# Kernel tuning notes

Measured on AMD Instinct MI355X. Metric: run time of the kernel, lower is better.

The kernel has to match this reference:

```python
import jax, jax.numpy as jnp
import numpy as np

B = 65536
NREQ = 2097152
NVEH = 1048576
NPAS = 2097152
E = 4194304


def _xavier(key, fi, fo):
    gain = 5.0 / 3.0  # tanh gain
    std = gain * np.sqrt(2.0 / (fi + fo))
    return jax.random.normal(key, (fi, fo), dtype=jnp.float32) * std


def scatter_mean(x, idx, num_segments):
    s = jax.ops.segment_sum(x, idx, num_segments=num_segments)
    c = jax.ops.segment_sum(jnp.ones((x.shape[0], 1), x.dtype), idx, num_segments=num_segments)
    return s / jnp.maximum(c, 1.0)


def setup_inputs() -> dict:
    key = jax.random.key(0)
    ks = jax.random.split(key, 16)
    inp = {
        "requests_x": jax.random.normal(ks[0], (NREQ, 10), dtype=jnp.float32),
        "requests_x_batch": jnp.sort(jax.random.randint(ks[1], (NREQ,), 0, B)),
        "vehicles_x": jax.random.normal(ks[2], (NVEH, 8), dtype=jnp.float32),
        "vehicles_x_batch": jnp.sort(jax.random.randint(ks[3], (NVEH,), 0, B)),
        "passengers_x": jax.random.normal(ks[4], (NPAS, 10), dtype=jnp.float32),
        "veh2pas_receiver_edge_index": jax.random.randint(ks[5], (E,), 0, NPAS),
        "veh2pas_sender_edge_index": jax.random.randint(ks[6], (E,), 0, NVEH),
        "req2veh_receiver_start_index": jax.random.randint(ks[7], (B,), 0, NVEH),
        "W_req": _xavier(ks[8], 10, 16), "b_req": jnp.zeros((16,), jnp.float32),
        "W_veh": _xavier(ks[9], 8, 16), "b_veh": jnp.zeros((16,), jnp.float32),
        "W_pas": _xavier(ks[10], 10, 16), "b_pas": jnp.zeros((16,), jnp.float32),
        "W1": _xavier(ks[11], 64, 64), "b1": jnp.zeros((64,), jnp.float32),
        "W2": _xavier(ks[12], 64, 64), "b2": jnp.zeros((64,), jnp.float32),
        "W3": _xavier(ks[13], 64, 1), "b3": jnp.zeros((1,), jnp.float32),
    }
    return inp


def reference(requests_x, requests_x_batch, vehicles_x, vehicles_x_batch, passengers_x,
              veh2pas_receiver_edge_index, veh2pas_sender_edge_index,
              req2veh_receiver_start_index,
              W_req, b_req, W_veh, b_veh, W_pas, b_pas, W1, b1, W2, b2, W3, b3):
    # per-node-type small MLPs
    req_feat = jnp.tanh(requests_x @ W_req + b_req)            # [NREQ,16]
    req_mean = scatter_mean(req_feat, requests_x_batch, B)      # [B,16]
    veh_feat = jnp.tanh(vehicles_x @ W_veh + b_veh)             # [NVEH,16]
    pas_feat = jnp.tanh(passengers_x @ W_pas + b_pas)           # [NPAS,16]
    # gather passengers along edges, mean-pool onto vehicles
    pas_mean = scatter_mean(pas_feat[veh2pas_receiver_edge_index],
                            veh2pas_sender_edge_index, NVEH)    # [NVEH,16]
    ego_feat = jnp.concatenate([veh_feat, pas_mean], axis=-1)[req2veh_receiver_start_index]  # [B,32]
    veh_mean = scatter_mean(veh_feat, vehicles_x_batch, B)      # [B,16]
    action_feat = jnp.concatenate([req_mean, ego_feat, veh_mean], axis=-1)  # [B,64]
    h = jnp.tanh(action_feat @ W1 + b1)
    h = jnp.tanh(h @ W2 + b2)
    return h @ W3 + b3                                          # [B,1]
```

## Files before the change

kernel.cpp:

```cpp
#include <hip/hip_runtime.h>
#include <cstddef>
#include <cstdint>

#define TPB 256
#define BATCH 65536
#define NREQ 2097152
#define NVEH 1048576
#define NEDGE 4194304
#define CAP 32
#define RSENT 0xFFFFu

__device__ __forceinline__ float fast_tanh(float x) {
    float e = __expf(2.0f * x);
    return fmaf(-2.0f, __builtin_amdgcn_rcpf(e + 1.0f), 1.0f);
}
__device__ __forceinline__ float4 tanh4(float4 v) {
    return make_float4(fast_tanh(v.x), fast_tanh(v.y), fast_tanh(v.z), fast_tanh(v.w));
}

template<int F>
__device__ __forceinline__ void load_row(const float* __restrict__ x, int r, float* xr) {
    if constexpr (F == 10) {
        const float2* p = reinterpret_cast<const float2*>(x + (size_t)r * 10);
        #pragma unroll
        for (int i = 0; i < 5; ++i) { float2 t = p[i]; xr[2*i] = t.x; xr[2*i+1] = t.y; }
    } else {
        const float4* p = reinterpret_cast<const float4*>(x + (size_t)r * 8);
        float4 a = p[0], b = p[1];
        xr[0]=a.x; xr[1]=a.y; xr[2]=a.z; xr[3]=a.w;
        xr[4]=b.x; xr[5]=b.y; xr[6]=b.z; xr[7]=b.w;
    }
}

__global__ __launch_bounds__(TPB) void k_bounds(
    const int* __restrict__ req_batch, const int* __restrict__ veh_batch,
    const int* __restrict__ req2veh,
    int* __restrict__ seg_req, int* __restrict__ seg_veh,
    unsigned* __restrict__ markbits, unsigned short* __restrict__ rank16,
    int* __restrict__ cnt)
{
    int t = blockIdx.x * TPB + threadIdx.x;
    int i0 = t * 4;
    {
        int4 c = *reinterpret_cast<const int4*>(req_batch + i0);
        int prev = (i0 == 0) ? -1 : req_batch[i0 - 1];
        int vals[4] = {c.x, c.y, c.z, c.w};
        #pragma unroll
        for (int u = 0; u < 4; ++u) {
            for (int b = prev + 1; b <= vals[u]; ++b) seg_req[b] = i0 + u;
            prev = vals[u];
        }
        if (i0 + 4 == NREQ)
            for (int b = prev + 1; b <= BATCH; ++b) seg_req[b] = NREQ;
    }
    if (i0 < NVEH) {
        int4 c = *reinterpret_cast<const int4*>(veh_batch + i0);
        int prev = (i0 == 0) ? -1 : veh_batch[i0 - 1];
        int vals[4] = {c.x, c.y, c.z, c.w};
        #pragma unroll
        for (int u = 0; u < 4; ++u) {
            for (int b = prev + 1; b <= vals[u]; ++b) seg_veh[b] = i0 + u;
            prev = vals[u];
        }
        if (i0 + 4 == NVEH)
            for (int b = prev + 1; b <= BATCH; ++b) seg_veh[b] = NVEH;
    }
    if (i0 < BATCH) {
        int4 vv = *reinterpret_cast<const int4*>(req2veh + i0);
        int vs[4] = {vv.x, vv.y, vv.z, vv.w};
        #pragma unroll
        for (int u = 0; u < 4; ++u) {
            int v = vs[u];
            unsigned bit = 1u << (v & 31);
            unsigned old = atomicOr(&markbits[v >> 5], bit);
            if (!(old & bit))
                rank16[v] = (unsigned short)atomicAdd(cnt, 1);
        }
    }
}

template<int F>
__device__ __forceinline__ void seg_mean_reg(
    const float* __restrict__ x, const int* __restrict__ seg,
    const float* __restrict__ W, const float* __restrict__ bias,
    float* __restrict__ mean_out, int b, int q)
{
    float4 wq[F];
    #pragma unroll
    for (int i = 0; i < F; ++i)
        wq[i] = *reinterpret_cast<const float4*>(&W[i*16 + q*4]);
    float4 bq = reinterpret_cast<const float4*>(bias)[q];

    int lo = seg[b];
    int hi = seg[b + 1];
    float4 s = make_float4(0.f, 0.f, 0.f, 0.f);

    int r = lo;
    for (; r + 4 <= hi; r += 4) {
        float xr[4][F];
        #pragma unroll
        for (int u = 0; u < 4; ++u) load_row<F>(x, r + u, xr[u]);
        #pragma unroll
        for (int u = 0; u < 4; ++u) {
            float4 acc = bq;
            #pragma unroll
            for (int i = 0; i < F; ++i) {
                acc.x = fmaf(xr[u][i], wq[i].x, acc.x);
                acc.y = fmaf(xr[u][i], wq[i].y, acc.y);
                acc.z = fmaf(xr[u][i], wq[i].z, acc.z);
                acc.w = fmaf(xr[u][i], wq[i].w, acc.w);
            }
            float4 tv = tanh4(acc);
            s.x += tv.x; s.y += tv.y; s.z += tv.z; s.w += tv.w;
        }
    }
    for (; r < hi; ++r) {
        float xr[F];
        load_row<F>(x, r, xr);
        float4 acc = bq;
        #pragma unroll
        for (int i = 0; i < F; ++i) {
            acc.x = fmaf(xr[i], wq[i].x, acc.x);
            acc.y = fmaf(xr[i], wq[i].y, acc.y);
            acc.z = fmaf(xr[i], wq[i].z, acc.z);
            acc.w = fmaf(xr[i], wq[i].w, acc.w);
        }
        float4 tv = tanh4(acc);
        s.x += tv.x; s.y += tv.y; s.z += tv.z; s.w += tv.w;
    }
    float inv = 1.0f / fmaxf((float)(hi - lo), 1.0f);
    float4 o = make_float4(s.x*inv, s.y*inv, s.z*inv, s.w*inv);
    reinterpret_cast<float4*>(mean_out)[(size_t)b*4 + q] = o;
}

__global__ __launch_bounds__(TPB, 4) void k_phase1(
    const float* __restrict__ requests_x, const int* __restrict__ seg_req,
    const float* __restrict__ vehicles_x, const int* __restrict__ seg_veh,
    const float* __restrict__ W_req, const float* __restrict__ b_req,
    const float* __restrict__ W_veh, const float* __restrict__ b_veh,
    float* __restrict__ req_mean, float* __restrict__ veh_mean)
{
    int blk = blockIdx.x, tid = threadIdx.x;
    if (blk < 1024) {
        int t = blk * TPB + tid;
        seg_mean_reg<10>(requests_x, seg_req, W_req, b_req, req_mean, t >> 2, t & 3);
    } else {
        int t = (blk - 1024) * TPB + tid;
        seg_mean_reg<8>(vehicles_x, seg_veh, W_veh, b_veh, veh_mean, t >> 2, t & 3);
    }
}

__global__ void k_edge(
    const int* __restrict__ send, const int* __restrict__ recv,
    const unsigned short* __restrict__ rank16,
    int* __restrict__ deg, int* __restrict__ bucket)
{
    int e4 = blockIdx.x * TPB + threadIdx.x;
    int4 sv = reinterpret_cast<const int4*>(send)[e4];
    int vv[4] = {sv.x, sv.y, sv.z, sv.w};
    unsigned rr[4];
    #pragma unroll
    for (int u = 0; u < 4; ++u) rr[u] = rank16[vv[u]];
    #pragma unroll
    for (int u = 0; u < 4; ++u) {
        if (rr[u] != RSENT) {
            int slot = atomicAdd(&deg[rr[u]], 1);
            if (slot < CAP) bucket[(size_t)rr[u] * CAP + slot] = recv[e4 * 4 + u];
        }
    }
}

__global__ __launch_bounds__(TPB, 3) void k_final(
    const float* __restrict__ req_mean, const float* __restrict__ veh_mean,
    const unsigned short* __restrict__ rank16, const int* __restrict__ deg,
    const int* __restrict__ bucket, const float* __restrict__ pas_x,
    const float* __restrict__ vehicles_x, const int* __restrict__ req2veh,
    const float* __restrict__ W_veh, const float* __restrict__ b_veh,
    const float* __restrict__ W_pas, const float* __restrict__ b_pas,
    const float* __restrict__ W1, const float* __restrict__ b1,
    const float* __restrict__ W2, const float* __restrict__ b2,
    const float* __restrict__ W3, const float* __restrict__ b3,
    float* __restrict__ out)
{
    __shared__ __align__(16) float sW1[4096];
    __shared__ __align__(16) float sW2[4096];
    __shared__ float sW3[64];
    __shared__ float sb1[64];
    __shared__ float sb2[64];

    int tid = threadIdx.x;
    {
        const float4* s1 = reinterpret_cast<const float4*>(W1);
        const float4* s2 = reinterpret_cast<const float4*>(W2);
        float4* d1 = reinterpret_cast<float4*>(sW1);
        float4* d2 = reinterpret_cast<float4*>(sW2);
        for (int i = tid; i < 1024; i += TPB) { d1[i] = s1[i]; d2[i] = s2[i]; }
        if (tid < 64) { sW3[tid] = W3[tid]; sb1[tid] = b1[tid]; sb2[tid] = b2[tid]; }
    }
    __syncthreads();

    int q = tid & 3;
    int b = blockIdx.x * (TPB / 4) + (tid >> 2);
    int lane = tid & 63;
    int lbase = lane & ~3;

    float a[64];
    {
        const float4* rs = reinterpret_cast<const float4*>(req_mean) + (size_t)b*4;
        const float4* vs = reinterpret_cast<const float4*>(veh_mean) + (size_t)b*4;
        #pragma unroll
        for (int j4 = 0; j4 < 4; ++j4) {
            float4 t = rs[j4];
            a[4*j4+0]=t.x; a[4*j4+1]=t.y; a[4*j4+2]=t.z; a[4*j4+3]=t.w;
            float4 u = vs[j4];
            a[48+4*j4+0]=u.x; a[48+4*j4+1]=u.y; a[48+4*j4+2]=u.z; a[48+4*j4+3]=u.w;
        }
    }
    int v = req2veh[b];

    float4 fv;
    {
        float4 wv[8];
        #pragma unroll
        for (int i = 0; i < 8; ++i)
            wv[i] = *reinterpret_cast<const float4*>(&W_veh[i*16 + q*4]);
        float4 bv = reinterpret_cast<const float4*>(b_veh)[q];
        const float4* vp = reinterpret_cast<const float4*>(vehicles_x + (size_t)v*8);
        float4 t0 = vp[0], t1 = vp[1];
        float vx[8] = {t0.x,t0.y,t0.z,t0.w,t1.x,t1.y,t1.z,t1.w};
        float4 acc = bv;
        #pragma unroll
        for (int i = 0; i < 8; ++i) {
            acc.x = fmaf(vx[i], wv[i].x, acc.x); acc.y = fmaf(vx[i], wv[i].y, acc.y);
            acc.z = fmaf(vx[i], wv[i].z, acc.z); acc.w = fmaf(vx[i], wv[i].w, acc.w);
        }
        fv = tanh4(acc);
    }

    float4 fp;
    {
        float4 wp[10];
        #pragma unroll
        for (int i = 0; i < 10; ++i)
            wp[i] = *reinterpret_cast<const float4*>(&W_pas[i*16 + q*4]);
        float4 bp = reinterpret_cast<const float4*>(b_pas)[q];
        int rk = rank16[v];
        int d = deg[rk];
        int n = min(d, CAP);
        const int4* bk4 = reinterpret_cast<const int4*>(bucket + (size_t)rk * CAP);
        float4 ps = make_float4(0.f, 0.f, 0.f, 0.f);
        for (int c = 0; c * 4 < n; ++c) {
            int4 idx = bk4[c];
            int pv[4] = {idx.x, idx.y, idx.z, idx.w};
            int m = n - c * 4;
            float px[4][10];
            #pragma unroll
            for (int u = 0; u < 4; ++u) {
                if (u < m) {
                    const float2* pp = reinterpret_cast<const float2*>(pas_x + (size_t)pv[u] * 10);
                    #pragma unroll
                    for (int i = 0; i < 5; ++i) {
                        float2 t = pp[i]; px[u][2*i] = t.x; px[u][2*i+1] = t.y;
                    }
                }
            }
            #pragma unroll
            for (int u = 0; u < 4; ++u) {
                if (u < m) {
                    float4 acc = bp;
                    #pragma unroll
                    for (int i = 0; i < 10; ++i) {
                        acc.x = fmaf(px[u][i], wp[i].x, acc.x);
                        acc.y = fmaf(px[u][i], wp[i].y, acc.y);
                        acc.z = fmaf(px[u][i], wp[i].z, acc.z);
                        acc.w = fmaf(px[u][i], wp[i].w, acc.w);
                    }
                    float4 t = tanh4(acc);
                    ps.x += t.x; ps.y += t.y; ps.z += t.z; ps.w += t.w;
                }
            }
        }
        float inv = 1.0f / fmaxf((float)d, 1.0f);
        fp = make_float4(ps.x*inv, ps.y*inv, ps.z*inv, ps.w*inv);
    }

    #pragma unroll
    for (int src = 0; src < 4; ++src) {
        a[16+4*src+0] = __shfl(fv.x, lbase+src);
        a[16+4*src+1] = __shfl(fv.y, lbase+src);
        a[16+4*src+2] = __shfl(fv.z, lbase+src);
        a[16+4*src+3] = __shfl(fv.w, lbase+src);
        a[32+4*src+0] = __shfl(fp.x, lbase+src);
        a[32+4*src+1] = __shfl(fp.y, lbase+src);
        a[32+4*src+2] = __shfl(fp.z, lbase+src);
        a[32+4*src+3] = __shfl(fp.w, lbase+src);
    }

    const float4* W1v = reinterpret_cast<const float4*>(sW1);
    const float4* W2v = reinterpret_cast<const float4*>(sW2);

    float hq[16];
    {
        float4 acc[4];
        #pragma unroll
        for (int jj = 0; jj < 4; ++jj)
            acc[jj] = *reinterpret_cast<const float4*>(&sb1[q*16 + jj*4]);
        #pragma unroll
        for (int k = 0; k < 64; ++k) {
            float ak = a[k];
            #pragma unroll
            for (int jj = 0; jj < 4; ++jj) {
                float4 w = W1v[k*16 + q*4 + jj];
                acc[jj].x = fmaf(ak, w.x, acc[jj].x); acc[jj].y = fmaf(ak, w.y, acc[jj].y);
                acc[jj].z = fmaf(ak, w.z, acc[jj].z); acc[jj].w = fmaf(ak, w.w, acc[jj].w);
            }
        }
        #pragma unroll
        for (int jj = 0; jj < 4; ++jj) {
            float4 t = tanh4(acc[jj]);
            hq[4*jj+0]=t.x; hq[4*jj+1]=t.y; hq[4*jj+2]=t.z; hq[4*jj+3]=t.w;
        }
    }
    #pragma unroll
    for (int src = 0; src < 4; ++src)
        #pragma unroll
        for (int jj = 0; jj < 16; ++jj)
            a[src*16 + jj] = __shfl(hq[jj], lbase + src);

    float o;
    {
        float4 acc[4];
        #pragma unroll
        for (int jj = 0; jj < 4; ++jj)
            acc[jj] = *reinterpret_cast<const float4*>(&sb2[q*16 + jj*4]);
        #pragma unroll
        for (int k = 0; k < 64; ++k) {
            float ak = a[k];
            #pragma unroll
            for (int jj = 0; jj < 4; ++jj) {
                float4 w = W2v[k*16 + q*4 + jj];
                acc[jj].x = fmaf(ak, w.x, acc[jj].x); acc[jj].y = fmaf(ak, w.y, acc[jj].y);
                acc[jj].z = fmaf(ak, w.z, acc[jj].z); acc[jj].w = fmaf(ak, w.w, acc[jj].w);
            }
        }
        o = 0.0f;
        #pragma unroll
        for (int jj = 0; jj < 4; ++jj) {
            float4 t = tanh4(acc[jj]);
            o = fmaf(t.x, sW3[q*16+4*jj+0], o);
            o = fmaf(t.y, sW3[q*16+4*jj+1], o);
            o = fmaf(t.z, sW3[q*16+4*jj+2], o);
            o = fmaf(t.w, sW3[q*16+4*jj+3], o);
        }
    }
    o += __shfl_xor(o, 1);
    o += __shfl_xor(o, 2);
    if (q == 0) out[b] = o + b3[0];
}

extern "C" void kernel_launch(void* const* d_in, const int* in_sizes, int n_in,
                              void* d_out, int out_size, void* d_ws, size_t ws_size,
                              hipStream_t stream) {
    const float* requests_x = (const float*)d_in[0];
    const int*   req_batch  = (const int*)d_in[1];
    const float* vehicles_x = (const float*)d_in[2];
    const int*   veh_batch  = (const int*)d_in[3];
    const float* pas_x      = (const float*)d_in[4];
    const int*   recv       = (const int*)d_in[5];
    const int*   send       = (const int*)d_in[6];
    const int*   req2veh    = (const int*)d_in[7];
    const float* W_req = (const float*)d_in[8];
    const float* b_req = (const float*)d_in[9];
    const float* W_veh = (const float*)d_in[10];
    const float* b_veh = (const float*)d_in[11];
    const float* W_pas = (const float*)d_in[12];
    const float* b_pas = (const float*)d_in[13];
    const float* W1 = (const float*)d_in[14];
    const float* b1 = (const float*)d_in[15];
    const float* W2 = (const float*)d_in[16];
    const float* b2 = (const float*)d_in[17];
    const float* W3 = (const float*)d_in[18];
    const float* b3 = (const float*)d_in[19];
    float* out = (float*)d_out;

    char* ws = (char*)d_ws;
    float*          req_mean = (float*)         (ws + 0);
    float*          veh_mean = (float*)         (ws + (4u<<20));
    int*            seg_req  = (int*)           (ws + (8u<<20));
    int*            seg_veh  = (int*)           (ws + (9u<<20));
    unsigned*       markbits = (unsigned*)      (ws + (10u<<20));
    int*            deg      = (int*)           (ws + (10u<<20) + (128u<<10));
    int*            cnt      = (int*)           (ws + (10u<<20) + (384u<<10));
    unsigned short* rank16   = (unsigned short*)(ws + (11u<<20));
    int*            bucket   = (int*)           (ws + (13u<<20));

    hipMemsetAsync(markbits, 0, (388u<<10), stream);
    hipMemsetAsync(rank16, 0xFF, NVEH * sizeof(unsigned short), stream);

    k_bounds<<<NREQ/4/TPB, TPB, 0, stream>>>(
        req_batch, veh_batch, req2veh, seg_req, seg_veh, markbits, rank16, cnt);

    k_edge<<<NEDGE/(TPB*4), TPB, 0, stream>>>(send, recv, rank16, deg, bucket);

    k_phase1<<<2048, TPB, 0, stream>>>(
        requests_x, seg_req, vehicles_x, seg_veh,
        W_req, b_req, W_veh, b_veh, req_mean, veh_mean);

    k_final<<<BATCH*4/TPB, TPB, 0, stream>>>(
        req_mean, veh_mean, rank16, deg, bucket, pas_x,
        vehicles_x, req2veh, W_veh, b_veh, W_pas, b_pas,
        W1, b1, W2, b2, W3, b3, out);
}
```

Baseline: 152.3 us.

## Compute passenger features in edge kernel and store half-precision features in buckets

```diff
diff --git a/kernel.cpp b/kernel.cpp
--- a/kernel.cpp
+++ b/kernel.cpp
@@ -1,4 +1,5 @@
 #include <hip/hip_runtime.h>
+#include <hip/hip_fp16.h>
 #include <cstddef>
 #include <cstdint>
 
@@ -152,20 +153,52 @@
 
 __global__ void k_edge(
     const int* __restrict__ send, const int* __restrict__ recv,
+    const float* __restrict__ pas_x,
+    const float* __restrict__ W_pas, const float* __restrict__ b_pas,
     const unsigned short* __restrict__ rank16,
-    int* __restrict__ deg, int* __restrict__ bucket)
+    int* __restrict__ deg, __half* __restrict__ bucketF)
 {
-    int e4 = blockIdx.x * TPB + threadIdx.x;
-    int4 sv = reinterpret_cast<const int4*>(send)[e4];
-    int vv[4] = {sv.x, sv.y, sv.z, sv.w};
-    unsigned rr[4];
+    int tid = threadIdx.x;
+    int lane = tid & 63;
+    int lbase = lane & ~3;
+    int q = tid & 3;
+
+    float4 wq[10];
     #pragma unroll
-    for (int u = 0; u < 4; ++u) rr[u] = rank16[vv[u]];
+    for (int i = 0; i < 10; ++i)
+        wq[i] = *reinterpret_cast<const float4*>(&W_pas[i*16 + q*4]);
+    float4 bq = reinterpret_cast<const float4*>(b_pas)[q];
+
+    int e = blockIdx.x * TPB + tid;
+    int v = send[e];
+    unsigned rk = rank16[v];
+    int slot = -1;
+    if (rk != RSENT) slot = atomicAdd(&deg[rk], 1);
+    int p = (rk != RSENT && slot < CAP) ? recv[e] : -1;
+
     #pragma unroll
     for (int u = 0; u < 4; ++u) {
-        if (rr[u] != RSENT) {
-            int slot = atomicAdd(&deg[rr[u]], 1);
-            if (slot < CAP) bucket[(size_t)rr[u] * CAP + slot] = recv[e4 * 4 + u];
+        int pu = __shfl(p, lbase + u);
+        if (pu >= 0) {
+            unsigned rku = (unsigned)__shfl((int)rk, lbase + u);
+            int slotu = __shfl(slot, lbase + u);
+            float px[10];
+            const float2* pp = reinterpret_cast<const float2*>(pas_x + (size_t)pu * 10);
+            #pragma unroll
+            for (int i = 0; i < 5; ++i) { float2 t = pp[i]; px[2*i] = t.x; px[2*i+1] = t.y; }
+            float4 acc = bq;
+            #pragma unroll
+            for (int i = 0; i < 10; ++i) {
+                acc.x = fmaf(px[i], wq[i].x, acc.x);
+                acc.y = fmaf(px[i], wq[i].y, acc.y);
+                acc.z = fmaf(px[i], wq[i].z, acc.z);
+                acc.w = fmaf(px[i], wq[i].w, acc.w);
+            }
+            float4 t = tanh4(acc);
+            __half2* dst = reinterpret_cast<__half2*>(
+                bucketF + ((size_t)rku * CAP + slotu) * 16) + q * 2;
+            dst[0] = __floats2half2_rn(t.x, t.y);
+            dst[1] = __floats2half2_rn(t.z, t.w);
         }
     }
 }
@@ -173,10 +206,9 @@
 __global__ __launch_bounds__(TPB, 3) void k_final(
     const float* __restrict__ req_mean, const float* __restrict__ veh_mean,
     const unsigned short* __restrict__ rank16, const int* __restrict__ deg,
-    const int* __restrict__ bucket, const float* __restrict__ pas_x,
+    const __half* __restrict__ bucketF,
     const float* __restrict__ vehicles_x, const int* __restrict__ req2veh,
     const float* __restrict__ W_veh, const float* __restrict__ b_veh,
-    const float* __restrict__ W_pas, const float* __restrict__ b_pas,
     const float* __restrict__ W1, const float* __restrict__ b1,
     const float* __restrict__ W2, const float* __restrict__ b2,
     const float* __restrict__ W3, const float* __restrict__ b3,
@@ -239,46 +271,19 @@
 
     float4 fp;
     {
-        float4 wp[10];
-        #pragma unroll
-        for (int i = 0; i < 10; ++i)
-            wp[i] = *reinterpret_cast<const float4*>(&W_pas[i*16 + q*4]);
-        float4 bp = reinterpret_cast<const float4*>(b_pas)[q];
         int rk = rank16[v];
         int d = deg[rk];
         int n = min(d, CAP);
-        const int4* bk4 = reinterpret_cast<const int4*>(bucket + (size_t)rk * CAP);
+        const __half2* base = reinterpret_cast<const __half2*>(
+            bucketF + (size_t)rk * CAP * 16) + q * 2;
         float4 ps = make_float4(0.f, 0.f, 0.f, 0.f);
-        for (int c = 0; c * 4 < n; ++c) {
-            int4 idx = bk4[c];
-            int pv[4] = {idx.x, idx.y, idx.z, idx.w};
-            int m = n - c * 4;
-            float px[4][10];
-            #pragma unroll
-            for (int u = 0; u < 4; ++u) {
-                if (u < m) {
-                    const float2* pp = reinterpret_cast<const float2*>(pas_x + (size_t)pv[u] * 10);
-                    #pragma unroll
-                    for (int i = 0; i < 5; ++i) {
-                        float2 t = pp[i]; px[u][2*i] = t.x; px[u][2*i+1] = t.y;
-                    }
-                }
-            }
-            #pragma unroll
-            for (int u = 0; u < 4; ++u) {
-                if (u < m) {
-                    float4 acc = bp;
-                    #pragma unroll
-                    for (int i = 0; i < 10; ++i) {
-                        acc.x = fmaf(px[u][i], wp[i].x, acc.x);
-                        acc.y = fmaf(px[u][i], wp[i].y, acc.y);
-                        acc.z = fmaf(px[u][i], wp[i].z, acc.z);
-                        acc.w = fmaf(px[u][i], wp[i].w, acc.w);
-                    }
-                    float4 t = tanh4(acc);
-                    ps.x += t.x; ps.y += t.y; ps.z += t.z; ps.w += t.w;
-                }
-            }
+        #pragma unroll 4
+        for (int s = 0; s < n; ++s) {
+            __half2 h0 = base[(size_t)s * 8 + 0];
+            __half2 h1 = base[(size_t)s * 8 + 1];
+            float2 f0 = __half22float2(h0);
+            float2 f1 = __half22float2(h1);
+            ps.x += f0.x; ps.y += f0.y; ps.z += f1.x; ps.w += f1.y;
         }
         float inv = 1.0f / fmaxf((float)d, 1.0f);
         fp = make_float4(ps.x*inv, ps.y*inv, ps.z*inv, ps.w*inv);
@@ -392,7 +397,7 @@
     int*            deg      = (int*)           (ws + (10u<<20) + (128u<<10));
     int*            cnt      = (int*)           (ws + (10u<<20) + (384u<<10));
     unsigned short* rank16   = (unsigned short*)(ws + (11u<<20));
-    int*            bucket   = (int*)           (ws + (13u<<20));
+    __half*         bucketF  = (__half*)        (ws + (13u<<20));
 
     hipMemsetAsync(markbits, 0, (388u<<10), stream);
     hipMemsetAsync(rank16, 0xFF, NVEH * sizeof(unsigned short), stream);
@@ -400,14 +405,15 @@
     k_bounds<<<NREQ/4/TPB, TPB, 0, stream>>>(
         req_batch, veh_batch, req2veh, seg_req, seg_veh, markbits, rank16, cnt);
 
-    k_edge<<<NEDGE/(TPB*4), TPB, 0, stream>>>(send, recv, rank16, deg, bucket);
+    k_edge<<<NEDGE/TPB, TPB, 0, stream>>>(
+        send, recv, pas_x, W_pas, b_pas, rank16, deg, bucketF);
 
     k_phase1<<<2048, TPB, 0, stream>>>(
         requests_x, seg_req, vehicles_x, seg_veh,
         W_req, b_req, W_veh, b_veh, req_mean, veh_mean);
 
     k_final<<<BATCH*4/TPB, TPB, 0, stream>>>(
-        req_mean, veh_mean, rank16, deg, bucket, pas_x,
-        vehicles_x, req2veh, W_veh, b_veh, W_pas, b_pas,
+        req_mean, veh_mean, rank16, deg, bucketF,
+        vehicles_x, req2veh, W_veh, b_veh,
         W1, b1, W2, b2, W3, b3, out);
 }
```

Result: slower. 162.2 us (+6.5%).
